# Kernel optimization log

Measured on AMD Instinct MI355X. Metric: run time of the kernel, lower is better.

## Reference

```python
import math
import jax, jax.numpy as jnp
import numpy as np

WS = [2048, 4096, 8192]
RS = [1, 2, 4]
HEAD_IDX = 0


def build_indices(n):
    """Static dilated gather indices: concat of every segment's strided slice.

    Matches _prepare_sparse_indices for the chosen (ws, rs, n), which yields
    zero padding (each segment contributes exactly max_subatt_n indices).
    """
    max_m = min(n, max(w // r for w, r in zip(WS, RS)))
    parts = []
    for w, r in zip(WS, RS):
        offset = HEAD_IDX % r
        for s in range(0, n, w):
            seg = np.arange(s, min(s + w, n))[offset::r]
            assert len(seg) == max_m, "config chosen to avoid padding"
            parts.append(seg)
    return np.concatenate(parts).astype(np.int32), max_m


def _forward(x, Wq, Wk, Wv):
    b, n, c = x.shape
    idx_np, m = build_indices(n)
    idx = jnp.asarray(idx_np)            # [S], S = num_subatt * m
    S = idx_np.shape[0]
    nb = S // m                          # number of sub-attention windows

    # gather -> [b, S, c] -> batched windows [b*nb, m, c]
    bx = x[:, idx, :].reshape(b * nb, m, c)

    # single-head causal attention on each window, also return softmax denoms
    scale = 1.0 / math.sqrt(c)
    q = bx @ Wq
    k = bx @ Wk
    v = bx @ Wv
    logits = jnp.einsum('bqc,bkc->bqk', q, k) * scale
    causal = jnp.tril(jnp.ones((m, m), dtype=bool))
    logits = jnp.where(causal, logits, -jnp.inf)
    lse = jax.scipy.special.logsumexp(logits, axis=-1)   # [b*nb, m]
    probs = jnp.exp(logits - lse[..., None])
    o = jnp.einsum('bqk,bkc->bqc', probs, v)             # [b*nb, m, c]
    denoms = jnp.exp(lse)                                 # softmax denominators

    o = o.reshape(b, S, c)
    denoms = denoms.reshape(b, S)

    # _mix_outputs: scatter-add denoms per target position, reweight, scatter-add outputs
    denom_sums = jnp.zeros((b, n), x.dtype).at[:, idx].add(denoms)
    alphas = denoms / denom_sums[:, idx]                  # [b, S]
    out = jnp.zeros((b, n, c), x.dtype).at[:, idx, :].add(o * alphas[..., None])
    return out


def setup_inputs() -> dict:
    key = jax.random.key(0)
    kx, kq, kk, kv = jax.random.split(key, 4)
    b, n, c = 4, 8192, 64
    s = 1.0 / math.sqrt(c)
    return {
        'x': jax.random.normal(kx, (b, n, c), dtype=jnp.float32),
        'Wq': jax.random.normal(kq, (c, c), dtype=jnp.float32) * s,
        'Wk': jax.random.normal(kk, (c, c), dtype=jnp.float32) * s,
        'Wv': jax.random.normal(kv, (c, c), dtype=jnp.float32) * s,
    }


def reference(x, Wq, Wk, Wv):
    return _forward(x, Wq, Wk, Wv)
```

## Files before the change

### kernel.cpp

```cpp
#include <hip/hip_runtime.h>
#include <math.h>

#define NB   4
#define NSEQ 8192
#define CDIM 64
#define M    2048
#define NW   7
#define NBLK2 72

typedef _Float16 half8 __attribute__((ext_vector_type(8)));
typedef __fp16 fp16x2 __attribute__((ext_vector_type(2)));
typedef float f32x4 __attribute__((ext_vector_type(4)));
typedef unsigned short u16x4 __attribute__((ext_vector_type(4)));

#if defined(__has_builtin) && __has_builtin(__builtin_amdgcn_exp2f)
#define EXP2(x) __builtin_amdgcn_exp2f(x)
#else
#define EXP2(x) __expf((x) * 0.69314718056f)
#endif

#define QSCALE 0.1803368801111204f
#define PBIAS 4.0f

#define K_OFF   0
#define VT_OFF  8192
#define VT_STRIDE 80
#define VT_BUF  5120

__device__ __forceinline__ int win_base(int w) {
    return (w < 4) ? (w << 11) : ((w < 6) ? ((w - 4) << 12) : 0);
}
__device__ __forceinline__ int win_stride(int w) {
    return (w < 4) ? 1 : ((w < 6) ? 2 : 4);
}

__global__ __launch_bounds__(256, 1) void qkv_proj(
        const float* __restrict__ x,
        const float* __restrict__ Wq, const float* __restrict__ Wk,
        const float* __restrict__ Wv,
        _Float16* __restrict__ Qg, _Float16* __restrict__ Kg,
        _Float16* __restrict__ Vg) {
    const int t = threadIdx.x;
    const int wid = t >> 6, lane = t & 63, l15 = lane & 15, quad = lane >> 4;

    half8 wb[3][2][4];
#pragma unroll
    for (int m = 0; m < 3; ++m) {
        const float* Wm = (m == 0) ? Wq : ((m == 1) ? Wk : Wv);
        const float sc = (m == 0) ? QSCALE : 1.0f;
#pragma unroll
        for (int kh = 0; kh < 2; ++kh)
#pragma unroll
            for (int nt = 0; nt < 4; ++nt) {
                float f[8];
#pragma unroll
                for (int j = 0; j < 8; ++j)
                    f[j] = Wm[(kh * 32 + quad * 8 + j) * 64 + nt * 16 + l15] * sc;
                union { fp16x2 h[4]; half8 v; } u;
#pragma unroll
                for (int p = 0; p < 4; ++p)
                    u.h[p] = __builtin_amdgcn_cvt_pkrtz(f[2 * p], f[2 * p + 1]);
                wb[m][kh][nt] = u.v;
            }
    }

    const int rowbase = blockIdx.x * 128 + wid * 32;
#pragma unroll
    for (int mt = 0; mt < 2; ++mt) {
        const int r0 = rowbase + mt * 16;
        half8 xa[2];
#pragma unroll
        for (int kh = 0; kh < 2; ++kh) {
            const float* xr = x + (size_t)(r0 + l15) * 64 + kh * 32 + quad * 8;
            const float4 a = *(const float4*)xr;
            const float4 b2 = *(const float4*)(xr + 4);
            union { fp16x2 h[4]; half8 v; } u;
            u.h[0] = __builtin_amdgcn_cvt_pkrtz(a.x, a.y);
            u.h[1] = __builtin_amdgcn_cvt_pkrtz(a.z, a.w);
            u.h[2] = __builtin_amdgcn_cvt_pkrtz(b2.x, b2.y);
            u.h[3] = __builtin_amdgcn_cvt_pkrtz(b2.z, b2.w);
            xa[kh] = u.v;
        }
#pragma unroll
        for (int m = 0; m < 3; ++m) {
            f32x4 acc[4];
#pragma unroll
            for (int nt = 0; nt < 4; ++nt) {
                acc[nt] = (f32x4){0.f, 0.f, 0.f, 0.f};
                acc[nt] = __builtin_amdgcn_mfma_f32_16x16x32_f16(xa[0], wb[m][0][nt], acc[nt], 0, 0, 0);
                acc[nt] = __builtin_amdgcn_mfma_f32_16x16x32_f16(xa[1], wb[m][1][nt], acc[nt], 0, 0, 0);
            }
            _Float16* outp = (m == 0) ? Qg : ((m == 1) ? Kg : Vg);
#pragma unroll
            for (int nt = 0; nt < 4; ++nt)
#pragma unroll
                for (int j = 0; j < 4; ++j)
                    outp[(size_t)(r0 + quad * 4 + j) * 64 + nt * 16 + l15] =
                        (_Float16)acc[nt][j];
        }
    }
}

__global__ __launch_bounds__(256, 4) void attn(
        const _Float16* __restrict__ Qg, const _Float16* __restrict__ Kg,
        const _Float16* __restrict__ Vg,
        _Float16* __restrict__ Op, float* __restrict__ Lp) {
    __shared__ __align__(16) char smem[18432];

    const int idx = (NBLK2 - 1) - (int)blockIdx.x;
    int QT = 0;
    QT += (idx >= 1);  QT += (idx >= 2);  QT += (idx >= 4);  QT += (idx >= 6);
    QT += (idx >= 9);  QT += (idx >= 12); QT += (idx >= 16); QT += (idx >= 20);
    QT += (idx >= 25); QT += (idx >= 30); QT += (idx >= 36); QT += (idx >= 42);
    QT += (idx >= 49); QT += (idx >= 56); QT += (idx >= 64);
    const int k2 = QT >> 1;
    const int cb = (QT & 1) ? (k2 + 1) * (k2 + 1) : k2 * (k2 + 1);
    const int ci = idx - cb;
    const int w = blockIdx.y, b = blockIdx.z;
    const int base = win_base(w), stride = win_stride(w);
    const int outblk = (b * NW + w) * NBLK2 + cb + ci;
    const int kt0 = ci * 8;
    const int ktmax = 4 * QT + 4;
    const int kt1 = (kt0 + 8 < ktmax) ? kt0 + 8 : ktmax;

    const _Float16* Qb = Qg + (size_t)b * NSEQ * 64;
    const _Float16* Kb = Kg + (size_t)b * NSEQ * 64;
    const _Float16* Vb = Vg + (size_t)b * NSEQ * 64;

    const int t = threadIdx.x;
    const int wid = t >> 6, lane = t & 63, l15 = lane & 15, quad = lane >> 4;

    const int sr = t >> 3, sch = t & 7;
    const int c4 = t & 15, kq = t >> 4;
    const int vd0 = 4 * c4;

    const size_t qr0 = (size_t)(base + stride * (QT * 128 + 16 * wid + l15)) * 64;
    const size_t qr1 = (size_t)(base + stride * (QT * 128 + 64 + 16 * wid + l15)) * 64;
    const half8 qa00 = *(const half8*)(Qb + qr0 + quad * 8);
    const half8 qa01 = *(const half8*)(Qb + qr0 + 32 + quad * 8);
    const half8 qa10 = *(const half8*)(Qb + qr1 + quad * 8);
    const half8 qa11 = *(const half8*)(Qb + qr1 + 32 + quad * 8);

    f32x4 oacc0[4], oacc1[4];
    float l0 = 0.f, l1 = 0.f;
#pragma unroll
    for (int ns = 0; ns < 4; ++ns) {
        oacc0[ns] = (f32x4){0.f, 0.f, 0.f, 0.f};
        oacc1[ns] = (f32x4){0.f, 0.f, 0.f, 0.f};
    }

    half8 pk;
    u16x4 pv0, pv1;

    {
        const size_t ka = (size_t)(base + stride * (kt0 * 32 + sr)) * 64 + sch * 8;
        pk = *(const half8*)(Kb + ka);
        const size_t va = (size_t)(base + stride * (kt0 * 32 + kq)) * 64 + vd0;
        pv0 = *(const u16x4*)(Vb + va);
        pv1 = *(const u16x4*)(Vb + va + (size_t)stride * 16 * 64);
        char* Kd = smem + K_OFF;
        char* Vd = smem + VT_OFF;
        *(half8*)(Kd + sr * 128 + ((sch ^ (sr & 7)) * 16)) = pk;
#pragma unroll
        for (int i = 0; i < 4; ++i) {
            int d = vd0 + i;
            unsigned int pkw = (unsigned int)pv0[i] | ((unsigned int)pv1[i] << 16);
            int ch = ((kq >> 2) ^ (d >> 4) ^ (d & 3) ^ ((d >> 2) & 3)) & 3;
            *(unsigned int*)(Vd + d * VT_STRIDE + ch * 16 + (kq & 3) * 4) = pkw;
        }
    }

    int cur = 0;
    for (int kt = kt0; kt < kt1; ++kt) {
        __syncthreads();
        const bool pf = (kt + 1 < kt1);
        if (pf) {
            const size_t ka = (size_t)(base + stride * ((kt + 1) * 32 + sr)) * 64 + sch * 8;
            pk = *(const half8*)(Kb + ka);
            const size_t va = (size_t)(base + stride * ((kt + 1) * 32 + kq)) * 64 + vd0;
            pv0 = *(const u16x4*)(Vb + va);
            pv1 = *(const u16x4*)(Vb + va + (size_t)stride * 16 * 64);
        }

        const char* Kd = smem + K_OFF + cur * 4096;
        const char* Vd = smem + VT_OFF + cur * VT_BUF;

        half8 kb[2][2];
#pragma unroll
        for (int ns = 0; ns < 2; ++ns) {
            const int krow = ns * 16 + l15, swk = krow & 7;
            kb[ns][0] = *(const half8*)(Kd + krow * 128 + ((quad ^ swk) * 16));
            kb[ns][1] = *(const half8*)(Kd + krow * 128 + (((quad + 4) ^ swk) * 16));
        }
        f32x4 sa0[2], sa1[2];
        __builtin_amdgcn_s_setprio(1);
#pragma unroll
        for (int ns = 0; ns < 2; ++ns) {
            f32x4 c0 = (f32x4){0.f, 0.f, 0.f, 0.f};
            c0 = __builtin_amdgcn_mfma_f32_16x16x32_f16(kb[ns][0], qa00, c0, 0, 0, 0);
            c0 = __builtin_amdgcn_mfma_f32_16x16x32_f16(kb[ns][1], qa01, c0, 0, 0, 0);
            sa0[ns] = c0;
            f32x4 c1 = (f32x4){0.f, 0.f, 0.f, 0.f};
            c1 = __builtin_amdgcn_mfma_f32_16x16x32_f16(kb[ns][0], qa10, c1, 0, 0, 0);
            c1 = __builtin_amdgcn_mfma_f32_16x16x32_f16(kb[ns][1], qa11, c1, 0, 0, 0);
            sa1[ns] = c1;
        }
        __builtin_amdgcn_s_setprio(0);
        if (kt >= 4 * QT) {
            const int q0 = QT * 128 + 16 * wid + l15 - kt * 32;
            const int kvb = quad * 4;
#pragma unroll
            for (int ns = 0; ns < 2; ++ns)
#pragma unroll
                for (int j = 0; j < 4; ++j) {
                    if (kvb + ns * 16 + j > q0)      sa0[ns][j] = -1e30f;
                    if (kvb + ns * 16 + j > q0 + 64) sa1[ns][j] = -1e30f;
                }
        }

        half8 vb[4];
#pragma unroll
        for (int ns = 0; ns < 4; ++ns) {
            const int d = ns * 16 + l15;
            const int ch = (quad ^ (d >> 4) ^ (d & 3) ^ ((d >> 2) & 3)) & 3;
            vb[ns] = *(const half8*)(Vd + d * VT_STRIDE + ch * 16);
        }

        {
            union { fp16x2 h[4]; half8 v; } pu;
#pragma unroll
            for (int u = 0; u < 4; ++u) {
                float pA = EXP2(sa0[0][u] - PBIAS);
                float pB = EXP2(sa0[1][u] - PBIAS);
                l0 += pA + pB;
                pu.h[u] = __builtin_amdgcn_cvt_pkrtz(pA, pB);
            }
            __builtin_amdgcn_s_setprio(1);
#pragma unroll
            for (int ns = 0; ns < 4; ++ns)
                oacc0[ns] = __builtin_amdgcn_mfma_f32_16x16x32_f16(pu.v, vb[ns], oacc0[ns], 0, 0, 0);
            __builtin_amdgcn_s_setprio(0);
        }
        {
            union { fp16x2 h[4]; half8 v; } pu;
#pragma unroll
            for (int u = 0; u < 4; ++u) {
                float pA = EXP2(sa1[0][u] - PBIAS);
                float pB = EXP2(sa1[1][u] - PBIAS);
                l1 += pA + pB;
                pu.h[u] = __builtin_amdgcn_cvt_pkrtz(pA, pB);
            }
            __builtin_amdgcn_s_setprio(1);
#pragma unroll
            for (int ns = 0; ns < 4; ++ns)
                oacc1[ns] = __builtin_amdgcn_mfma_f32_16x16x32_f16(pu.v, vb[ns], oacc1[ns], 0, 0, 0);
            __builtin_amdgcn_s_setprio(0);
        }

        if (pf) {
            char* Kn = smem + K_OFF + (cur ^ 1) * 4096;
            char* Vn = smem + VT_OFF + (cur ^ 1) * VT_BUF;
            *(half8*)(Kn + sr * 128 + ((sch ^ (sr & 7)) * 16)) = pk;
#pragma unroll
            for (int i = 0; i < 4; ++i) {
                int d = vd0 + i;
                unsigned int pkw = (unsigned int)pv0[i] | ((unsigned int)pv1[i] << 16);
                int ch = ((kq >> 2) ^ (d >> 4) ^ (d & 3) ^ ((d >> 2) & 3)) & 3;
                *(unsigned int*)(Vn + d * VT_STRIDE + ch * 16 + (kq & 3) * 4) = pkw;
            }
        }
        cur ^= 1;
    }

    l0 += __shfl_xor(l0, 16, 64);
    l0 += __shfl_xor(l0, 32, 64);
    l1 += __shfl_xor(l1, 16, 64);
    l1 += __shfl_xor(l1, 32, 64);
    if (quad == 0) {
        Lp[(size_t)outblk * 128 + 16 * wid + l15]      = l0;
        Lp[(size_t)outblk * 128 + 64 + 16 * wid + l15] = l1;
    }
    const int qrow0 = 16 * wid + quad * 4;
#pragma unroll
    for (int j = 0; j < 4; ++j) {
        const float inv0 = 1.0f / __shfl(l0, quad * 4 + j, 64);
        const float inv1 = 1.0f / __shfl(l1, quad * 4 + j, 64);
        const size_t r0off = ((size_t)outblk * 128 + qrow0 + j) * 64 + l15;
        const size_t r1off = ((size_t)outblk * 128 + 64 + qrow0 + j) * 64 + l15;
#pragma unroll
        for (int ns = 0; ns < 4; ++ns) {
            Op[r0off + ns * 16] = (_Float16)(oacc0[ns][j] * inv0);
            Op[r1off + ns * 16] = (_Float16)(oacc1[ns][j] * inv1);
        }
    }
}

typedef _Float16 half8v __attribute__((ext_vector_type(8)));
__global__ __launch_bounds__(256) void mix_out(
        const _Float16* __restrict__ Op, const float* __restrict__ Lp,
        float* __restrict__ out) {
    int gid = blockIdx.x * 256 + threadIdx.x;
    int f8 = gid & 7;
    int tpos = (gid >> 3) & (NSEQ - 1);
    int b = gid >> 16;

    float wsum = 0.f;
    float acc[8];
#pragma unroll
    for (int k = 0; k < 8; ++k) acc[k] = 0.f;

    {
        int w = tpos >> 11, j = tpos & (M - 1);
        int QT = j >> 7, q = j & 127, k2 = QT >> 1;
        int cbase = (QT & 1) ? (k2 + 1) * (k2 + 1) : k2 * (k2 + 1);
        int bb = ((b * NW + w) * NBLK2 + cbase) * 128 + q;
        int cmax = j >> 8;
#pragma unroll
        for (int c = 0; c < 8; ++c) {
            int cc = (c <= cmax) ? c : cmax;
            int ix = bb + cc * 128;
            float li = Lp[ix];
            li = (c <= cmax) ? li : 0.f;
            half8v v = *(const half8v*)(Op + (size_t)ix * 64 + f8 * 8);
            wsum += li;
#pragma unroll
            for (int k = 0; k < 8; ++k) acc[k] += li * (float)v[k];
        }
    }
    if (!(tpos & 1)) {
        int w = 4 + (tpos >> 12), j = (tpos & 4095) >> 1;
        int QT = j >> 7, q = j & 127, k2 = QT >> 1;
        int cbase = (QT & 1) ? (k2 + 1) * (k2 + 1) : k2 * (k2 + 1);
        int bb = ((b * NW + w) * NBLK2 + cbase) * 128 + q;
        int cmax = j >> 8;
#pragma unroll
        for (int c = 0; c < 8; ++c) {
            int cc = (c <= cmax) ? c : cmax;
            int ix = bb + cc * 128;
            float li = Lp[ix];
            li = (c <= cmax) ? li : 0.f;
            half8v v = *(const half8v*)(Op + (size_t)ix * 64 + f8 * 8);
            wsum += li;
#pragma unroll
            for (int k = 0; k < 8; ++k) acc[k] += li * (float)v[k];
        }
    }
    if (!(tpos & 3)) {
        int j = tpos >> 2;
        int QT = j >> 7, q = j & 127, k2 = QT >> 1;
        int cbase = (QT & 1) ? (k2 + 1) * (k2 + 1) : k2 * (k2 + 1);
        int bb = ((b * NW + 6) * NBLK2 + cbase) * 128 + q;
        int cmax = j >> 8;
#pragma unroll
        for (int c = 0; c < 8; ++c) {
            int cc = (c <= cmax) ? c : cmax;
            int ix = bb + cc * 128;
            float li = Lp[ix];
            li = (c <= cmax) ? li : 0.f;
            half8v v = *(const half8v*)(Op + (size_t)ix * 64 + f8 * 8);
            wsum += li;
#pragma unroll
            for (int k = 0; k < 8; ++k) acc[k] += li * (float)v[k];
        }
    }

    float inv = 1.0f / wsum;
    size_t o = ((size_t)b * NSEQ + tpos) * 64 + f8 * 8;
    float4 r0 = make_float4(acc[0] * inv, acc[1] * inv, acc[2] * inv, acc[3] * inv);
    float4 r1 = make_float4(acc[4] * inv, acc[5] * inv, acc[6] * inv, acc[7] * inv);
    *(float4*)&out[o] = r0;
    *(float4*)&out[o + 4] = r1;
}

extern "C" void kernel_launch(void* const* d_in, const int* in_sizes, int n_in,
                              void* d_out, int out_size, void* d_ws, size_t ws_size,
                              hipStream_t stream) {
    const float* x  = (const float*)d_in[0];
    const float* Wq = (const float*)d_in[1];
    const float* Wk = (const float*)d_in[2];
    const float* Wv = (const float*)d_in[3];
    float* out = (float*)d_out;

    const size_t QN = (size_t)NB * NSEQ * CDIM;
    _Float16* Qg = (_Float16*)d_ws;
    _Float16* Kg = Qg + QN;
    _Float16* Vg = Kg + QN;
    _Float16* Op = Vg + QN;
    float* Lp   = (float*)(Op + (size_t)NB * NW * NBLK2 * 128 * 64);

    qkv_proj<<<NB * NSEQ / 128, 256, 0, stream>>>(x, Wq, Wk, Wv, Qg, Kg, Vg);
    attn<<<dim3(NBLK2, NW, NB), 256, 0, stream>>>(Qg, Kg, Vg, Op, Lp);
    mix_out<<<(NB * NSEQ * 8) / 256, 256, 0, stream>>>(Op, Lp, out);
}
```

Before: 110.7 us.

## Load K tiles directly into registers and unroll attention loop by two

K fragments for the QK^T MFMA are now loaded straight from global memory into registers, one tile ahead, instead of being staged through swizzled shared memory. Only V still goes through LDS, which shrinks the LDS footprint from 18 KB to 10 KB. The loop is unrolled by two with templated buffer indices so register double-buffering of K needs no dynamic indexing. The cost is more global load traffic per wave, since each wave reads K itself, plus higher register pressure. The step count per block is always a multiple of two here, so the unroll by two stays in bounds.

Result: slower. 198.0 us (+78.8%).

```diff
diff --git a/kernel.cpp b/kernel.cpp
--- a/kernel.cpp
+++ b/kernel.cpp
@@ -22,8 +22,6 @@
 #define QSCALE 0.1803368801111204f
 #define PBIAS 4.0f
 
-#define K_OFF   0
-#define VT_OFF  8192
 #define VT_STRIDE 80
 #define VT_BUF  5120
 
@@ -101,11 +99,125 @@
     }
 }
 
+struct AttnState {
+    const _Float16* Qb; const _Float16* Kb; const _Float16* Vb;
+    int base, stride, QT, kt1;
+    int wid, l15, quad, kq, vd0;
+    half8 qa00, qa01, qa10, qa11;
+    f32x4 oacc0[4], oacc1[4];
+    float l0, l1;
+    u16x4 pv0, pv1;
+    char* smem;
+};
+
+__device__ __forceinline__ void loadK(AttnState& s, half8 kb[2][2], int kt) {
+#pragma unroll
+    for (int ns = 0; ns < 2; ++ns) {
+        const size_t kr =
+            (size_t)(s.base + s.stride * (kt * 32 + ns * 16 + s.l15)) * 64;
+        kb[ns][0] = *(const half8*)(s.Kb + kr + s.quad * 8);
+        kb[ns][1] = *(const half8*)(s.Kb + kr + 32 + s.quad * 8);
+    }
+}
+
+__device__ __forceinline__ void loadV(AttnState& s, int kt) {
+    const size_t va = (size_t)(s.base + s.stride * (kt * 32 + s.kq)) * 64 + s.vd0;
+    s.pv0 = *(const u16x4*)(s.Vb + va);
+    s.pv1 = *(const u16x4*)(s.Vb + va + (size_t)s.stride * 16 * 64);
+}
+
+template <int CUR>
+__device__ __forceinline__ void writeV(AttnState& s) {
+    char* Vn = s.smem + CUR * VT_BUF;
+#pragma unroll
+    for (int i = 0; i < 4; ++i) {
+        int d = s.vd0 + i;
+        unsigned int pkw = (unsigned int)s.pv0[i] | ((unsigned int)s.pv1[i] << 16);
+        int ch = ((s.kq >> 2) ^ (d >> 4) ^ (d & 3) ^ ((d >> 2) & 3)) & 3;
+        *(unsigned int*)(Vn + d * VT_STRIDE + ch * 16 + (s.kq & 3) * 4) = pkw;
+    }
+}
+
+template <int CUR>
+__device__ __forceinline__ void stepAttn(AttnState& s, int kt,
+                                         half8 kbC[2][2], half8 kbN[2][2]) {
+    const bool pf = (kt + 1 < s.kt1);
+    if (pf) {
+        loadK(s, kbN, kt + 1);
+        loadV(s, kt + 1);
+    }
+    const char* Vd = s.smem + CUR * VT_BUF;
+    half8 vb[4];
+#pragma unroll
+    for (int ns = 0; ns < 4; ++ns) {
+        const int d = ns * 16 + s.l15;
+        const int ch = (s.quad ^ (d >> 4) ^ (d & 3) ^ ((d >> 2) & 3)) & 3;
+        vb[ns] = *(const half8*)(Vd + d * VT_STRIDE + ch * 16);
+    }
+    f32x4 sa0[2], sa1[2];
+    __builtin_amdgcn_s_setprio(1);
+#pragma unroll
+    for (int ns = 0; ns < 2; ++ns) {
+        f32x4 c0 = (f32x4){0.f, 0.f, 0.f, 0.f};
+        c0 = __builtin_amdgcn_mfma_f32_16x16x32_f16(kbC[ns][0], s.qa00, c0, 0, 0, 0);
+        c0 = __builtin_amdgcn_mfma_f32_16x16x32_f16(kbC[ns][1], s.qa01, c0, 0, 0, 0);
+        sa0[ns] = c0;
+        f32x4 c1 = (f32x4){0.f, 0.f, 0.f, 0.f};
+        c1 = __builtin_amdgcn_mfma_f32_16x16x32_f16(kbC[ns][0], s.qa10, c1, 0, 0, 0);
+        c1 = __builtin_amdgcn_mfma_f32_16x16x32_f16(kbC[ns][1], s.qa11, c1, 0, 0, 0);
+        sa1[ns] = c1;
+    }
+    __builtin_amdgcn_s_setprio(0);
+    if (kt >= 4 * s.QT) {
+        const int q0 = s.QT * 128 + 16 * s.wid + s.l15 - kt * 32;
+        const int kvb = s.quad * 4;
+#pragma unroll
+        for (int ns = 0; ns < 2; ++ns)
+#pragma unroll
+            for (int j = 0; j < 4; ++j) {
+                if (kvb + ns * 16 + j > q0)      sa0[ns][j] = -1e30f;
+                if (kvb + ns * 16 + j > q0 + 64) sa1[ns][j] = -1e30f;
+            }
+    }
+    {
+        union { fp16x2 h[4]; half8 v; } pu;
+#pragma unroll
+        for (int u = 0; u < 4; ++u) {
+            float pA = EXP2(sa0[0][u] - PBIAS);
+            float pB = EXP2(sa0[1][u] - PBIAS);
+            s.l0 += pA + pB;
+            pu.h[u] = __builtin_amdgcn_cvt_pkrtz(pA, pB);
+        }
+        __builtin_amdgcn_s_setprio(1);
+#pragma unroll
+        for (int ns = 0; ns < 4; ++ns)
+            s.oacc0[ns] = __builtin_amdgcn_mfma_f32_16x16x32_f16(pu.v, vb[ns], s.oacc0[ns], 0, 0, 0);
+        __builtin_amdgcn_s_setprio(0);
+    }
+    {
+        union { fp16x2 h[4]; half8 v; } pu;
+#pragma unroll
+        for (int u = 0; u < 4; ++u) {
+            float pA = EXP2(sa1[0][u] - PBIAS);
+            float pB = EXP2(sa1[1][u] - PBIAS);
+            s.l1 += pA + pB;
+            pu.h[u] = __builtin_amdgcn_cvt_pkrtz(pA, pB);
+        }
+        __builtin_amdgcn_s_setprio(1);
+#pragma unroll
+        for (int ns = 0; ns < 4; ++ns)
+            s.oacc1[ns] = __builtin_amdgcn_mfma_f32_16x16x32_f16(pu.v, vb[ns], s.oacc1[ns], 0, 0, 0);
+        __builtin_amdgcn_s_setprio(0);
+    }
+    if (pf) writeV<CUR ^ 1>(s);
+    __syncthreads();
+}
+
 __global__ __launch_bounds__(256, 4) void attn(
         const _Float16* __restrict__ Qg, const _Float16* __restrict__ Kg,
         const _Float16* __restrict__ Vg,
         _Float16* __restrict__ Op, float* __restrict__ Lp) {
-    __shared__ __align__(16) char smem[18432];
+    __shared__ __align__(16) char smem[10240];
 
     const int idx = (NBLK2 - 1) - (int)blockIdx.x;
     int QT = 0;
@@ -123,155 +235,45 @@
     const int ktmax = 4 * QT + 4;
     const int kt1 = (kt0 + 8 < ktmax) ? kt0 + 8 : ktmax;
 
-    const _Float16* Qb = Qg + (size_t)b * NSEQ * 64;
-    const _Float16* Kb = Kg + (size_t)b * NSEQ * 64;
-    const _Float16* Vb = Vg + (size_t)b * NSEQ * 64;
-
     const int t = threadIdx.x;
     const int wid = t >> 6, lane = t & 63, l15 = lane & 15, quad = lane >> 4;
 
-    const int sr = t >> 3, sch = t & 7;
-    const int c4 = t & 15, kq = t >> 4;
-    const int vd0 = 4 * c4;
+    AttnState s;
+    s.Qb = Qg + (size_t)b * NSEQ * 64;
+    s.Kb = Kg + (size_t)b * NSEQ * 64;
+    s.Vb = Vg + (size_t)b * NSEQ * 64;
+    s.base = base; s.stride = stride; s.QT = QT; s.kt1 = kt1;
+    s.wid = wid; s.l15 = l15; s.quad = quad;
+    s.kq = t >> 4; s.vd0 = 4 * (t & 15);
+    s.smem = smem;
+    s.l0 = 0.f; s.l1 = 0.f;
 
     const size_t qr0 = (size_t)(base + stride * (QT * 128 + 16 * wid + l15)) * 64;
     const size_t qr1 = (size_t)(base + stride * (QT * 128 + 64 + 16 * wid + l15)) * 64;
-    const half8 qa00 = *(const half8*)(Qb + qr0 + quad * 8);
-    const half8 qa01 = *(const half8*)(Qb + qr0 + 32 + quad * 8);
-    const half8 qa10 = *(const half8*)(Qb + qr1 + quad * 8);
-    const half8 qa11 = *(const half8*)(Qb + qr1 + 32 + quad * 8);
-
-    f32x4 oacc0[4], oacc1[4];
-    float l0 = 0.f, l1 = 0.f;
+    s.qa00 = *(const half8*)(s.Qb + qr0 + quad * 8);
+    s.qa01 = *(const half8*)(s.Qb + qr0 + 32 + quad * 8);
+    s.qa10 = *(const half8*)(s.Qb + qr1 + quad * 8);
+    s.qa11 = *(const half8*)(s.Qb + qr1 + 32 + quad * 8);
+
 #pragma unroll
     for (int ns = 0; ns < 4; ++ns) {
-        oacc0[ns] = (f32x4){0.f, 0.f, 0.f, 0.f};
-        oacc1[ns] = (f32x4){0.f, 0.f, 0.f, 0.f};
-    }
-
-    half8 pk;
-    u16x4 pv0, pv1;
-
-    {
-        const size_t ka = (size_t)(base + stride * (kt0 * 32 + sr)) * 64 + sch * 8;
-        pk = *(const half8*)(Kb + ka);
-        const size_t va = (size_t)(base + stride * (kt0 * 32 + kq)) * 64 + vd0;
-        pv0 = *(const u16x4*)(Vb + va);
-        pv1 = *(const u16x4*)(Vb + va + (size_t)stride * 16 * 64);
-        char* Kd = smem + K_OFF;
-        char* Vd = smem + VT_OFF;
-        *(half8*)(Kd + sr * 128 + ((sch ^ (sr & 7)) * 16)) = pk;
-#pragma unroll
-        for (int i = 0; i < 4; ++i) {
-            int d = vd0 + i;
-            unsigned int pkw = (unsigned int)pv0[i] | ((unsigned int)pv1[i] << 16);
-            int ch = ((kq >> 2) ^ (d >> 4) ^ (d & 3) ^ ((d >> 2) & 3)) & 3;
-            *(unsigned int*)(Vd + d * VT_STRIDE + ch * 16 + (kq & 3) * 4) = pkw;
-        }
-    }
-
-    int cur = 0;
-    for (int kt = kt0; kt < kt1; ++kt) {
-        __syncthreads();
-        const bool pf = (kt + 1 < kt1);
-        if (pf) {
-            const size_t ka = (size_t)(base + stride * ((kt + 1) * 32 + sr)) * 64 + sch * 8;
-            pk = *(const half8*)(Kb + ka);
-            const size_t va = (size_t)(base + stride * ((kt + 1) * 32 + kq)) * 64 + vd0;
-            pv0 = *(const u16x4*)(Vb + va);
-            pv1 = *(const u16x4*)(Vb + va + (size_t)stride * 16 * 64);
-        }
-
-        const char* Kd = smem + K_OFF + cur * 4096;
-        const char* Vd = smem + VT_OFF + cur * VT_BUF;
-
-        half8 kb[2][2];
-#pragma unroll
-        for (int ns = 0; ns < 2; ++ns) {
-            const int krow = ns * 16 + l15, swk = krow & 7;
-            kb[ns][0] = *(const half8*)(Kd + krow * 128 + ((quad ^ swk) * 16));
-            kb[ns][1] = *(const half8*)(Kd + krow * 128 + (((quad + 4) ^ swk) * 16));
-        }
-        f32x4 sa0[2], sa1[2];
-        __builtin_amdgcn_s_setprio(1);
-#pragma unroll
-        for (int ns = 0; ns < 2; ++ns) {
-            f32x4 c0 = (f32x4){0.f, 0.f, 0.f, 0.f};
-            c0 = __builtin_amdgcn_mfma_f32_16x16x32_f16(kb[ns][0], qa00, c0, 0, 0, 0);
-            c0 = __builtin_amdgcn_mfma_f32_16x16x32_f16(kb[ns][1], qa01, c0, 0, 0, 0);
-            sa0[ns] = c0;
-            f32x4 c1 = (f32x4){0.f, 0.f, 0.f, 0.f};
-            c1 = __builtin_amdgcn_mfma_f32_16x16x32_f16(kb[ns][0], qa10, c1, 0, 0, 0);
-            c1 = __builtin_amdgcn_mfma_f32_16x16x32_f16(kb[ns][1], qa11, c1, 0, 0, 0);
-            sa1[ns] = c1;
-        }
-        __builtin_amdgcn_s_setprio(0);
-        if (kt >= 4 * QT) {
-            const int q0 = QT * 128 + 16 * wid + l15 - kt * 32;
-            const int kvb = quad * 4;
-#pragma unroll
-            for (int ns = 0; ns < 2; ++ns)
-#pragma unroll
-                for (int j = 0; j < 4; ++j) {
-                    if (kvb + ns * 16 + j > q0)      sa0[ns][j] = -1e30f;
-                    if (kvb + ns * 16 + j > q0 + 64) sa1[ns][j] = -1e30f;
-                }
-        }
-
-        half8 vb[4];
-#pragma unroll
-        for (int ns = 0; ns < 4; ++ns) {
-            const int d = ns * 16 + l15;
-            const int ch = (quad ^ (d >> 4) ^ (d & 3) ^ ((d >> 2) & 3)) & 3;
-            vb[ns] = *(const half8*)(Vd + d * VT_STRIDE + ch * 16);
-        }
-
-        {
-            union { fp16x2 h[4]; half8 v; } pu;
-#pragma unroll
-            for (int u = 0; u < 4; ++u) {
-                float pA = EXP2(sa0[0][u] - PBIAS);
-                float pB = EXP2(sa0[1][u] - PBIAS);
-                l0 += pA + pB;
-                pu.h[u] = __builtin_amdgcn_cvt_pkrtz(pA, pB);
-            }
-            __builtin_amdgcn_s_setprio(1);
-#pragma unroll
-            for (int ns = 0; ns < 4; ++ns)
-                oacc0[ns] = __builtin_amdgcn_mfma_f32_16x16x32_f16(pu.v, vb[ns], oacc0[ns], 0, 0, 0);
-            __builtin_amdgcn_s_setprio(0);
-        }
-        {
-            union { fp16x2 h[4]; half8 v; } pu;
-#pragma unroll
-            for (int u = 0; u < 4; ++u) {
-                float pA = EXP2(sa1[0][u] - PBIAS);
-                float pB = EXP2(sa1[1][u] - PBIAS);
-                l1 += pA + pB;
-                pu.h[u] = __builtin_amdgcn_cvt_pkrtz(pA, pB);
-            }
-            __builtin_amdgcn_s_setprio(1);
-#pragma unroll
-            for (int ns = 0; ns < 4; ++ns)
-                oacc1[ns] = __builtin_amdgcn_mfma_f32_16x16x32_f16(pu.v, vb[ns], oacc1[ns], 0, 0, 0);
-            __builtin_amdgcn_s_setprio(0);
-        }
-
-        if (pf) {
-            char* Kn = smem + K_OFF + (cur ^ 1) * 4096;
-            char* Vn = smem + VT_OFF + (cur ^ 1) * VT_BUF;
-            *(half8*)(Kn + sr * 128 + ((sch ^ (sr & 7)) * 16)) = pk;
-#pragma unroll
-            for (int i = 0; i < 4; ++i) {
-                int d = vd0 + i;
-                unsigned int pkw = (unsigned int)pv0[i] | ((unsigned int)pv1[i] << 16);
-                int ch = ((kq >> 2) ^ (d >> 4) ^ (d & 3) ^ ((d >> 2) & 3)) & 3;
-                *(unsigned int*)(Vn + d * VT_STRIDE + ch * 16 + (kq & 3) * 4) = pkw;
-            }
-        }
-        cur ^= 1;
-    }
-
+        s.oacc0[ns] = (f32x4){0.f, 0.f, 0.f, 0.f};
+        s.oacc1[ns] = (f32x4){0.f, 0.f, 0.f, 0.f};
+    }
+
+    half8 kbA[2][2], kbB[2][2];
+
+    loadK(s, kbA, kt0);
+    loadV(s, kt0);
+    writeV<0>(s);
+    __syncthreads();
+
+    for (int kt = kt0; kt < kt1; kt += 2) {
+        stepAttn<0>(s, kt,     kbA, kbB);
+        stepAttn<1>(s, kt + 1, kbB, kbA);
+    }
+
+    float l0 = s.l0, l1 = s.l1;
     l0 += __shfl_xor(l0, 16, 64);
     l0 += __shfl_xor(l0, 32, 64);
     l1 += __shfl_xor(l1, 16, 64);
@@ -289,8 +291,8 @@
         const size_t r1off = ((size_t)outblk * 128 + 64 + qrow0 + j) * 64 + l15;
 #pragma unroll
         for (int ns = 0; ns < 4; ++ns) {
-            Op[r0off + ns * 16] = (_Float16)(oacc0[ns][j] * inv0);
-            Op[r1off + ns * 16] = (_Float16)(oacc1[ns][j] * inv1);
+            Op[r0off + ns * 16] = (_Float16)(s.oacc0[ns][j] * inv0);
+            Op[r1off + ns * 16] = (_Float16)(s.oacc1[ns][j] * inv1);
         }
     }
 }
```

## Load K fragments straight into registers and double-buffer them across unrolled steps

Applied to the files above, without the earlier changes.

The K tile is no longer staged through shared memory. Each wave now loads its MFMA K operands directly from global memory into one of two register sets, which alternate across a loop unrolled by two. Only the transposed V tile still goes through LDS, so the shared buffer shrinks and the per-step K LDS writes and reads disappear. The cost is that all four waves fetch the same K rows from global memory, four times the K traffic through the caches, and the larger register footprint may hurt scheduling.

New measurement: 195.9 us. +76.9%, slower.

```diff
diff --git a/kernel.cpp b/kernel.cpp
--- a/kernel.cpp
+++ b/kernel.cpp
@@ -22,8 +22,6 @@
 #define QSCALE 0.1803368801111204f
 #define PBIAS 4.0f
 
-#define K_OFF   0
-#define VT_OFF  8192
 #define VT_STRIDE 80
 #define VT_BUF  5120
 
@@ -105,7 +103,7 @@
         const _Float16* __restrict__ Qg, const _Float16* __restrict__ Kg,
         const _Float16* __restrict__ Vg,
         _Float16* __restrict__ Op, float* __restrict__ Lp) {
-    __shared__ __align__(16) char smem[18432];
+    __shared__ __align__(16) char smem[10240];
 
     const int idx = (NBLK2 - 1) - (int)blockIdx.x;
     int QT = 0;
@@ -130,7 +128,6 @@
     const int t = threadIdx.x;
     const int wid = t >> 6, lane = t & 63, l15 = lane & 15, quad = lane >> 4;
 
-    const int sr = t >> 3, sch = t & 7;
     const int c4 = t & 15, kq = t >> 4;
     const int vd0 = 4 * c4;
 
@@ -149,127 +146,124 @@
         oacc1[ns] = (f32x4){0.f, 0.f, 0.f, 0.f};
     }
 
-    half8 pk;
+    half8 kbA[2][2], kbB[2][2];
     u16x4 pv0, pv1;
 
-    {
-        const size_t ka = (size_t)(base + stride * (kt0 * 32 + sr)) * 64 + sch * 8;
-        pk = *(const half8*)(Kb + ka);
-        const size_t va = (size_t)(base + stride * (kt0 * 32 + kq)) * 64 + vd0;
-        pv0 = *(const u16x4*)(Vb + va);
-        pv1 = *(const u16x4*)(Vb + va + (size_t)stride * 16 * 64);
-        char* Kd = smem + K_OFF;
-        char* Vd = smem + VT_OFF;
-        *(half8*)(Kd + sr * 128 + ((sch ^ (sr & 7)) * 16)) = pk;
-#pragma unroll
-        for (int i = 0; i < 4; ++i) {
-            int d = vd0 + i;
-            unsigned int pkw = (unsigned int)pv0[i] | ((unsigned int)pv1[i] << 16);
-            int ch = ((kq >> 2) ^ (d >> 4) ^ (d & 3) ^ ((d >> 2) & 3)) & 3;
-            *(unsigned int*)(Vd + d * VT_STRIDE + ch * 16 + (kq & 3) * 4) = pkw;
-        }
-    }
-
-    int cur = 0;
-    for (int kt = kt0; kt < kt1; ++kt) {
-        __syncthreads();
-        const bool pf = (kt + 1 < kt1);
-        if (pf) {
-            const size_t ka = (size_t)(base + stride * ((kt + 1) * 32 + sr)) * 64 + sch * 8;
-            pk = *(const half8*)(Kb + ka);
-            const size_t va = (size_t)(base + stride * ((kt + 1) * 32 + kq)) * 64 + vd0;
-            pv0 = *(const u16x4*)(Vb + va);
-            pv1 = *(const u16x4*)(Vb + va + (size_t)stride * 16 * 64);
-        }
-
-        const char* Kd = smem + K_OFF + cur * 4096;
-        const char* Vd = smem + VT_OFF + cur * VT_BUF;
-
-        half8 kb[2][2];
-#pragma unroll
-        for (int ns = 0; ns < 2; ++ns) {
-            const int krow = ns * 16 + l15, swk = krow & 7;
-            kb[ns][0] = *(const half8*)(Kd + krow * 128 + ((quad ^ swk) * 16));
-            kb[ns][1] = *(const half8*)(Kd + krow * 128 + (((quad + 4) ^ swk) * 16));
-        }
-        f32x4 sa0[2], sa1[2];
-        __builtin_amdgcn_s_setprio(1);
-#pragma unroll
-        for (int ns = 0; ns < 2; ++ns) {
-            f32x4 c0 = (f32x4){0.f, 0.f, 0.f, 0.f};
-            c0 = __builtin_amdgcn_mfma_f32_16x16x32_f16(kb[ns][0], qa00, c0, 0, 0, 0);
-            c0 = __builtin_amdgcn_mfma_f32_16x16x32_f16(kb[ns][1], qa01, c0, 0, 0, 0);
-            sa0[ns] = c0;
-            f32x4 c1 = (f32x4){0.f, 0.f, 0.f, 0.f};
-            c1 = __builtin_amdgcn_mfma_f32_16x16x32_f16(kb[ns][0], qa10, c1, 0, 0, 0);
-            c1 = __builtin_amdgcn_mfma_f32_16x16x32_f16(kb[ns][1], qa11, c1, 0, 0, 0);
-            sa1[ns] = c1;
-        }
-        __builtin_amdgcn_s_setprio(0);
-        if (kt >= 4 * QT) {
-            const int q0 = QT * 128 + 16 * wid + l15 - kt * 32;
-            const int kvb = quad * 4;
-#pragma unroll
-            for (int ns = 0; ns < 2; ++ns)
-#pragma unroll
-                for (int j = 0; j < 4; ++j) {
-                    if (kvb + ns * 16 + j > q0)      sa0[ns][j] = -1e30f;
-                    if (kvb + ns * 16 + j > q0 + 64) sa1[ns][j] = -1e30f;
-                }
-        }
-
-        half8 vb[4];
-#pragma unroll
-        for (int ns = 0; ns < 4; ++ns) {
-            const int d = ns * 16 + l15;
-            const int ch = (quad ^ (d >> 4) ^ (d & 3) ^ ((d >> 2) & 3)) & 3;
-            vb[ns] = *(const half8*)(Vd + d * VT_STRIDE + ch * 16);
-        }
-
-        {
-            union { fp16x2 h[4]; half8 v; } pu;
-#pragma unroll
-            for (int u = 0; u < 4; ++u) {
-                float pA = EXP2(sa0[0][u] - PBIAS);
-                float pB = EXP2(sa0[1][u] - PBIAS);
-                l0 += pA + pB;
-                pu.h[u] = __builtin_amdgcn_cvt_pkrtz(pA, pB);
-            }
-            __builtin_amdgcn_s_setprio(1);
-#pragma unroll
-            for (int ns = 0; ns < 4; ++ns)
-                oacc0[ns] = __builtin_amdgcn_mfma_f32_16x16x32_f16(pu.v, vb[ns], oacc0[ns], 0, 0, 0);
-            __builtin_amdgcn_s_setprio(0);
-        }
-        {
-            union { fp16x2 h[4]; half8 v; } pu;
-#pragma unroll
-            for (int u = 0; u < 4; ++u) {
-                float pA = EXP2(sa1[0][u] - PBIAS);
-                float pB = EXP2(sa1[1][u] - PBIAS);
-                l1 += pA + pB;
-                pu.h[u] = __builtin_amdgcn_cvt_pkrtz(pA, pB);
-            }
-            __builtin_amdgcn_s_setprio(1);
-#pragma unroll
-            for (int ns = 0; ns < 4; ++ns)
-                oacc1[ns] = __builtin_amdgcn_mfma_f32_16x16x32_f16(pu.v, vb[ns], oacc1[ns], 0, 0, 0);
-            __builtin_amdgcn_s_setprio(0);
-        }
-
-        if (pf) {
-            char* Kn = smem + K_OFF + (cur ^ 1) * 4096;
-            char* Vn = smem + VT_OFF + (cur ^ 1) * VT_BUF;
-            *(half8*)(Kn + sr * 128 + ((sch ^ (sr & 7)) * 16)) = pk;
-#pragma unroll
-            for (int i = 0; i < 4; ++i) {
-                int d = vd0 + i;
-                unsigned int pkw = (unsigned int)pv0[i] | ((unsigned int)pv1[i] << 16);
-                int ch = ((kq >> 2) ^ (d >> 4) ^ (d & 3) ^ ((d >> 2) & 3)) & 3;
-                *(unsigned int*)(Vn + d * VT_STRIDE + ch * 16 + (kq & 3) * 4) = pkw;
-            }
-        }
-        cur ^= 1;
+#define LOADK(kb, kt)                                                        \
+    {                                                                        \
+        _Pragma("unroll")                                                    \
+        for (int ns = 0; ns < 2; ++ns) {                                     \
+            const size_t kr =                                                \
+                (size_t)(base + stride * ((kt) * 32 + ns * 16 + l15)) * 64;  \
+            kb[ns][0] = *(const half8*)(Kb + kr + quad * 8);                 \
+            kb[ns][1] = *(const half8*)(Kb + kr + 32 + quad * 8);            \
+        }                                                                    \
+    }
+
+#define LOADV(kt)                                                            \
+    {                                                                        \
+        const size_t va =                                                    \
+            (size_t)(base + stride * ((kt) * 32 + kq)) * 64 + vd0;           \
+        pv0 = *(const u16x4*)(Vb + va);                                      \
+        pv1 = *(const u16x4*)(Vb + va + (size_t)stride * 16 * 64);           \
+    }
+
+#define WRITEV(cur)                                                          \
+    {                                                                        \
+        char* Vn = smem + (cur) * VT_BUF;                                    \
+        _Pragma("unroll")                                                    \
+        for (int i = 0; i < 4; ++i) {                                        \
+            int d = vd0 + i;                                                 \
+            unsigned int pkw =                                               \
+                (unsigned int)pv0[i] | ((unsigned int)pv1[i] << 16);         \
+            int ch = ((kq >> 2) ^ (d >> 4) ^ (d & 3) ^ ((d >> 2) & 3)) & 3;  \
+            *(unsigned int*)(Vn + d * VT_STRIDE + ch * 16 + (kq & 3) * 4) =  \
+                pkw;                                                         \
+        }                                                                    \
+    }
+
+    LOADK(kbA, kt0);
+    LOADV(kt0);
+    WRITEV(0);
+    __syncthreads();
+
+#define STEP(kt, kbC, kbN, cur)                                              \
+    {                                                                        \
+        const bool pf = ((kt) + 1 < kt1);                                    \
+        if (pf) {                                                            \
+            LOADK(kbN, (kt) + 1);                                            \
+            LOADV((kt) + 1);                                                 \
+        }                                                                    \
+        const char* Vd = smem + (cur) * VT_BUF;                              \
+        half8 vb[4];                                                         \
+        _Pragma("unroll")                                                    \
+        for (int ns = 0; ns < 4; ++ns) {                                     \
+            const int d = ns * 16 + l15;                                     \
+            const int ch = (quad ^ (d >> 4) ^ (d & 3) ^ ((d >> 2) & 3)) & 3; \
+            vb[ns] = *(const half8*)(Vd + d * VT_STRIDE + ch * 16);          \
+        }                                                                    \
+        f32x4 sa0[2], sa1[2];                                                \
+        __builtin_amdgcn_s_setprio(1);                                       \
+        _Pragma("unroll")                                                    \
+        for (int ns = 0; ns < 2; ++ns) {                                     \
+            f32x4 c0 = (f32x4){0.f, 0.f, 0.f, 0.f};                          \
+            c0 = __builtin_amdgcn_mfma_f32_16x16x32_f16(kbC[ns][0], qa00, c0, 0, 0, 0); \
+            c0 = __builtin_amdgcn_mfma_f32_16x16x32_f16(kbC[ns][1], qa01, c0, 0, 0, 0); \
+            sa0[ns] = c0;                                                    \
+            f32x4 c1 = (f32x4){0.f, 0.f, 0.f, 0.f};                          \
+            c1 = __builtin_amdgcn_mfma_f32_16x16x32_f16(kbC[ns][0], qa10, c1, 0, 0, 0); \
+            c1 = __builtin_amdgcn_mfma_f32_16x16x32_f16(kbC[ns][1], qa11, c1, 0, 0, 0); \
+            sa1[ns] = c1;                                                    \
+        }                                                                    \
+        __builtin_amdgcn_s_setprio(0);                                       \
+        if ((kt) >= 4 * QT) {                                                \
+            const int q0 = QT * 128 + 16 * wid + l15 - (kt) * 32;            \
+            const int kvb = quad * 4;                                        \
+            _Pragma("unroll")                                                \
+            for (int ns = 0; ns < 2; ++ns)                                   \
+                _Pragma("unroll")                                            \
+                for (int j = 0; j < 4; ++j) {                                \
+                    if (kvb + ns * 16 + j > q0)      sa0[ns][j] = -1e30f;    \
+                    if (kvb + ns * 16 + j > q0 + 64) sa1[ns][j] = -1e30f;    \
+                }                                                            \
+        }                                                                    \
+        {                                                                    \
+            union { fp16x2 h[4]; half8 v; } pu;                              \
+            _Pragma("unroll")                                                \
+            for (int u = 0; u < 4; ++u) {                                    \
+                float pA = EXP2(sa0[0][u] - PBIAS);                          \
+                float pB = EXP2(sa0[1][u] - PBIAS);                          \
+                l0 += pA + pB;                                               \
+                pu.h[u] = __builtin_amdgcn_cvt_pkrtz(pA, pB);                \
+            }                                                                \
+            __builtin_amdgcn_s_setprio(1);                                   \
+            _Pragma("unroll")                                                \
+            for (int ns = 0; ns < 4; ++ns)                                   \
+                oacc0[ns] = __builtin_amdgcn_mfma_f32_16x16x32_f16(pu.v, vb[ns], oacc0[ns], 0, 0, 0); \
+            __builtin_amdgcn_s_setprio(0);                                   \
+        }                                                                    \
+        {                                                                    \
+            union { fp16x2 h[4]; half8 v; } pu;                              \
+            _Pragma("unroll")                                                \
+            for (int u = 0; u < 4; ++u) {                                    \
+                float pA = EXP2(sa1[0][u] - PBIAS);                          \
+                float pB = EXP2(sa1[1][u] - PBIAS);                          \
+                l1 += pA + pB;                                               \
+                pu.h[u] = __builtin_amdgcn_cvt_pkrtz(pA, pB);                \
+            }                                                                \
+            __builtin_amdgcn_s_setprio(1);                                   \
+            _Pragma("unroll")                                                \
+            for (int ns = 0; ns < 4; ++ns)                                   \
+                oacc1[ns] = __builtin_amdgcn_mfma_f32_16x16x32_f16(pu.v, vb[ns], oacc1[ns], 0, 0, 0); \
+            __builtin_amdgcn_s_setprio(0);                                   \
+        }                                                                    \
+        if (pf) WRITEV((cur) ^ 1);                                           \
+        __syncthreads();                                                     \
+    }
+
+    for (int kt = kt0; kt < kt1; kt += 2) {
+        STEP(kt,     kbA, kbB, 0);
+        STEP(kt + 1, kbB, kbA, 1);
     }
 
     l0 += __shfl_xor(l0, 16, 64);
```
